# Optimization experiments

Measured on AMD Instinct MI355X. Metric: run time of the kernel, lower is better.

## Reference

```python
import jax, jax.numpy as jnp
import numpy as np

B, S, DMODEL, NHEAD = 2, 2048, 1024, 16
DK = DMODEL // NHEAD
INITRANGE = 0.1


def setup_inputs() -> dict:
    key = jax.random.key(0)
    kq, kk, kv, kwq, kwk, kwv, kwo = jax.random.split(key, 7)
    unif = lambda k, shape: jax.random.uniform(k, shape, jnp.float32, -INITRANGE, INITRANGE)
    return {
        "Q": jax.random.normal(kq, (B, S, DMODEL), jnp.float32),
        "K": jax.random.normal(kk, (B, S, DMODEL), jnp.float32),
        "V": jax.random.normal(kv, (B, S, DMODEL), jnp.float32),
        "WQ": unif(kwq, (NHEAD, DMODEL, DK)),
        "WK": unif(kwk, (NHEAD, DMODEL, DK)),
        "WV": unif(kwv, (NHEAD, DMODEL, DK)),
        "WO": unif(kwo, (NHEAD * DK, DMODEL)),
    }


def reference(Q, K, V, WQ, WK, WV, WO):
    dk = WQ.shape[-1]
    # per-head projections: [B,S,D] x [H,D,dk] -> [B,H,S,dk]
    Qi = jnp.einsum('bsd,hdk->bhsk', Q, WQ)
    Ki = jnp.einsum('bsd,hdk->bhsk', K, WK)
    Vi = jnp.einsum('bsd,hdk->bhsk', V, WV)
    scale = 1.0 / jnp.sqrt(jnp.asarray(dk, Qi.dtype))
    # full attention matrix [B,H,S,S] (faithful to the hand-rolled module; dropout in eval mode)
    attn = jax.nn.softmax(jnp.einsum('bhsk,bhtk->bhst', Qi, Ki) * scale, axis=-1)
    headi = jnp.einsum('bhst,bhtk->bhsk', attn, Vi)  # [B,H,S,dk]
    b, h, s, _ = headi.shape
    # NOTE: original does a raw reshape of contiguous (B,H,S,dk) -> (B,S,H*dk),
    # which mixes head and sequence axes in memory order. jnp row-major reshape
    # reproduces exactly the same element layout.
    out = headi.reshape(b, s, h * dk) @ WO  # [B,S,DMODEL]
    return out
```

## Files before the change

### kernel.cpp

```cpp
#include <hip/hip_runtime.h>
#include <hip/hip_bf16.h>
#include <stdint.h>

typedef unsigned short u16;
typedef unsigned int u32;
typedef __attribute__((ext_vector_type(4))) float f32x4;
typedef __attribute__((ext_vector_type(16))) float f32x16;
typedef __attribute__((ext_vector_type(8))) short bf16x8;
typedef __attribute__((ext_vector_type(4))) unsigned int u32x4;
typedef __attribute__((ext_vector_type(2))) unsigned int u32x2;

#define DEV __device__ __forceinline__

DEV u16 f2bf(float f) {
  union { float f; uint32_t u; } v; v.f = f;
  uint32_t u = v.u;
  return (u16)((u + 0x7fffu + ((u >> 16) & 1u)) >> 16);
}
DEV float bf2f(u16 h) {
  union { uint32_t u; float f; } v; v.u = ((uint32_t)h) << 16;
  return v.f;
}

DEV u32 cvtpk(float a, float b) {
  u32 r;
  asm("v_cvt_pk_bf16_f32 %0, %1, %2" : "=v"(r) : "v"(a), "v"(b));
  return r;
}

DEV void plswap(u32& a, u32& b) {
  asm("v_permlane32_swap_b32 %0, %1" : "+v"(a), "+v"(b));
}

DEV float fexp2(float x) {
  float r;
  asm("v_exp_f32 %0, %1" : "=v"(r) : "v"(x));
  return r;
}

DEV void gload_lds16(const u16* g, u16* l) {
  __builtin_amdgcn_global_load_lds(
      (const __attribute__((address_space(1))) void*)g,
      (__attribute__((address_space(3))) void*)l, 16, 0, 0);
}

__global__ __launch_bounds__(256) void prep_kernel(
    const float* __restrict__ Q, const float* __restrict__ K, const float* __restrict__ V,
    u16* __restrict__ Qb, u16* __restrict__ Kb, u16* __restrict__ Vb) {
  const int i = blockIdx.x * 256 + threadIdx.x;
#pragma unroll
  for (int it = 0; it < 3; ++it) {
    int idx = it * 1048576 + i;
    int which = idx >> 20, j = idx & 1048575;
    const float* src = which == 0 ? Q : (which == 1 ? K : V);
    u16* dst = which == 0 ? Qb : (which == 1 ? Kb : Vb);
    float4 v = ((const float4*)src)[j];
    u32x2 pk;
    pk[0] = (u32)f2bf(v.x) | ((u32)f2bf(v.y) << 16);
    pk[1] = (u32)f2bf(v.z) | ((u32)f2bf(v.w) << 16);
    *(u32x2*)(dst + (size_t)j * 4) = pk;
  }
}

__global__ __launch_bounds__(256) void transposeW_kernel(
    const float* __restrict__ WQ, const float* __restrict__ WK, const float* __restrict__ WV,
    const float* __restrict__ WO, u16* __restrict__ Wt, u16* __restrict__ Wot) {
  __shared__ __align__(16) u16 tl[64][72];
  const int tid = threadIdx.x;
  const int bid = blockIdx.x;
  const float* src;
  u16* dst;
  int rstride;
  if (bid < 768) {
    int p = bid >> 8, rest = bid & 255;
    int h = rest >> 4, dt = rest & 15;
    const float* W = p == 0 ? WQ : (p == 1 ? WK : WV);
    src = W + (size_t)(h * 1024 + dt * 64) * 64;
    dst = Wt + (size_t)p * 1048576 + (size_t)h * 64 * 1024 + dt * 64;
    rstride = 64;
  } else {
    int idx2 = bid - 768;
    int kt = idx2 >> 4, ct = idx2 & 15;
    src = WO + (size_t)kt * 64 * 1024 + ct * 64;
    dst = Wot + (size_t)ct * 64 * 1024 + kt * 64;
    rstride = 1024;
  }
#pragma unroll
  for (int i = 0; i < 2; ++i) {
    int idx = i * 256 + tid;
    int row = idx >> 3, c8 = idx & 7;
    const float* sp = src + (size_t)row * rstride + c8 * 8;
    float4 a = *(const float4*)sp;
    float4 b = *(const float4*)(sp + 4);
    u32x4 pk;
    pk[0] = (u32)f2bf(a.x) | ((u32)f2bf(a.y) << 16);
    pk[1] = (u32)f2bf(a.z) | ((u32)f2bf(a.w) << 16);
    pk[2] = (u32)f2bf(b.x) | ((u32)f2bf(b.y) << 16);
    pk[3] = (u32)f2bf(b.z) | ((u32)f2bf(b.w) << 16);
    *(u32x4*)&tl[row][c8 * 8] = pk;
  }
  __syncthreads();
#pragma unroll
  for (int i = 0; i < 2; ++i) {
    int idx = i * 256 + tid;
    int row2 = idx >> 3, s8 = idx & 7;
    u32x4 outv;
    u16* tp = (u16*)&outv;
#pragma unroll
    for (int j = 0; j < 8; ++j) tp[j] = tl[s8 * 8 + j][row2];
    *(u32x4*)(dst + (size_t)row2 * 1024 + s8 * 8) = outv;
  }
}

template <int OUT_BF16>
__global__ __launch_bounds__(256, 3) void gemm_kernel(const u16* __restrict__ A,
                                                      const u16* __restrict__ Bt,
                                                      void* __restrict__ Cout) {
  __shared__ __align__(16) u16 Alds[128 * 64];
  __shared__ __align__(16) u16 Blds[128 * 64];
  const size_t zo = blockIdx.z;
  A += zo * 4194304;
  Bt += zo * 1048576;
  const int tid = threadIdx.x;
  const int l = tid & 63, w = tid >> 6;
  const int wm = w >> 1, wn = w & 1;
  const int d = blockIdx.x + 32 * blockIdx.y;
  const int orig = (d & 7) * 32 + (d >> 3);
  const int tileM = (orig & 31) * 128, tileN = (orig >> 5) * 128;
  const int lr = l >> 3, lch = l & 7;

  f32x4 acc[4][4] = {};

  for (int kt = 0; kt < 16; ++kt) {
    const int k0 = kt * 64;
#pragma unroll
    for (int i = 0; i < 4; ++i) {
      int r = i * 32 + w * 8 + lr;
      int sch = lch ^ (r & 7);
      gload_lds16(A + (size_t)(tileM + r) * 1024 + k0 + sch * 8, Alds + i * 2048 + w * 512);
      gload_lds16(Bt + (size_t)(tileN + r) * 1024 + k0 + sch * 8, Blds + i * 2048 + w * 512);
    }
    __syncthreads();
    bf16x8 af[4][2], bfr[4][2];
#pragma unroll
    for (int m = 0; m < 4; ++m) {
#pragma unroll
      for (int kk = 0; kk < 2; ++kk) {
        int row = wm * 64 + m * 16 + (l & 15);
        int ch = ((l >> 4) + kk * 4) ^ (row & 7);
        af[m][kk] = *(const bf16x8*)(Alds + row * 64 + ch * 8);
        int rowb = wn * 64 + m * 16 + (l & 15);
        int chb = ((l >> 4) + kk * 4) ^ (rowb & 7);
        bfr[m][kk] = *(const bf16x8*)(Blds + rowb * 64 + chb * 8);
      }
    }
#pragma unroll
    for (int m = 0; m < 4; ++m)
#pragma unroll
      for (int n = 0; n < 4; ++n)
#pragma unroll
        for (int kk = 0; kk < 2; ++kk)
          acc[m][n] = __builtin_amdgcn_mfma_f32_16x16x32_bf16(af[m][kk], bfr[n][kk], acc[m][n], 0, 0, 0);
    __syncthreads();
  }
#pragma unroll
  for (int m = 0; m < 4; ++m) {
    int row0 = tileM + wm * 64 + m * 16 + ((l >> 4) << 2);
#pragma unroll
    for (int n = 0; n < 4; ++n) {
      int col = tileN + wn * 64 + n * 16 + (l & 15);
#pragma unroll
      for (int q = 0; q < 4; ++q) {
        if (OUT_BF16)
          ((u16*)Cout)[zo * 4194304 + (size_t)(row0 + q) * 1024 + col] = f2bf(acc[m][n][q]);
        else
          ((float*)Cout)[(size_t)(row0 + q) * 1024 + col] = acc[m][n][q];
      }
    }
  }
}

__global__ __launch_bounds__(256) void transposeV_kernel(const u16* __restrict__ Vi,
                                                         u16* __restrict__ Vt) {
  __shared__ __align__(16) u16 tl[64][72];
  const int tid = threadIdx.x;
  const int st = blockIdx.x * 64;
  const int bh = blockIdx.y;
  const int b = bh >> 4, h = bh & 15;
#pragma unroll
  for (int i = 0; i < 2; ++i) {
    int idx = i * 256 + tid;
    int s = idx >> 3, ch = idx & 7;
    const u16* src = Vi + (size_t)(b * 2048 + st + s) * 1024 + h * 64 + ch * 8;
    u32x2 a = *(const u32x2*)src;
    u32x2 bb = *(const u32x2*)(src + 4);
    *(u32x2*)&tl[s][ch * 8] = a;
    *(u32x2*)&tl[s][ch * 8 + 4] = bb;
  }
  __syncthreads();
#pragma unroll
  for (int i = 0; i < 2; ++i) {
    int idx = i * 256 + tid;
    int dk = idx >> 3, ch = idx & 7;
    u32x4 outv;
    u16* tp = (u16*)&outv;
#pragma unroll
    for (int j = 0; j < 8; ++j) tp[j] = tl[ch * 8 + j][dk];
    *(u32x4*)(Vt + ((size_t)bh * 64 + dk) * 2048 + st + ch * 8) = outv;
  }
}

__global__ __launch_bounds__(256, 4) void attn_kernel(const u16* __restrict__ Qi,
                                                      const u16* __restrict__ Ki,
                                                      const u16* __restrict__ Vt,
                                                      u16* __restrict__ Op,
                                                      float* __restrict__ Lp) {
  __shared__ __align__(16) u16 Kl[2][4096];
  __shared__ __align__(16) u16 Vl[2][4096];
  const int tid = threadIdx.x;
  const int l = tid & 63, w = tid >> 6;
  const int lq = l & 31, hi = l >> 5;
  const int lr = l >> 3, lch = l & 7;
  const int dd = blockIdx.x;
  const int orig = (dd & 7) * 128 + (dd >> 3);
  const int bh = orig >> 5;
  const int rem = orig & 31;
  const int qb = rem >> 1, kvh = rem & 1;
  const int b = bh >> 4, h = bh & 15;
  const int qt = qb * 128 + w * 32;
  const int tb = kvh * 1024;

  const u16* Kbase = Ki + (size_t)b * 2048 * 1024 + h * 64;
  const u16* Vbase = Vt + (size_t)bh * 64 * 2048;

  bf16x8 qf[4];
  {
    const u16* qp = Qi + (size_t)(b * 2048 + qt + lq) * 1024 + h * 64 + hi * 8;
#pragma unroll
    for (int s = 0; s < 4; ++s) {
      u32x4 t4 = *(const u32x4*)(qp + s * 16);
      u16* tp = (u16*)&t4;
#pragma unroll
      for (int j = 0; j < 8; ++j) tp[j] = f2bf(bf2f(tp[j]) * 0.1803368867f);
      qf[s] = *(bf16x8*)&t4;
    }
  }

  f32x16 o0 = {}, o1 = {};
  float l_r = 0.f;

  auto STAGE = [&](int bb, int t) {
#pragma unroll
    for (int i = 0; i < 2; ++i) {
      int r = i * 32 + w * 8 + lr;
      int sch = lch ^ (r & 7);
      gload_lds16(Kbase + (size_t)(tb + t * 64 + r) * 1024 + sch * 8,
                  Kl[bb] + i * 2048 + w * 512);
      gload_lds16(Vbase + (size_t)r * 2048 + tb + t * 64 + sch * 8,
                  Vl[bb] + i * 2048 + w * 512);
    }
  };

  STAGE(0, 0);

#pragma unroll 2
  for (int tile = 0; tile < 16; ++tile) {
    const int cur = tile & 1;
    __syncthreads();
    if (tile + 1 < 16) STAGE(cur ^ 1, tile + 1);
    const u16* kl = Kl[cur];
    const u16* vl = Vl[cur];

    f32x16 s0 = {}, s1 = {};
    __builtin_amdgcn_s_setprio(1);
#pragma unroll
    for (int s = 0; s < 4; ++s) {
      int row = lq, c = s * 2 + hi;
      bf16x8 kf = *(const bf16x8*)(kl + row * 64 + (c ^ (row & 7)) * 8);
      s0 = __builtin_amdgcn_mfma_f32_32x32x16_bf16(kf, qf[s], s0, 0, 0, 0);
    }
#pragma unroll
    for (int s = 0; s < 4; ++s) {
      int row = 32 + lq, c = s * 2 + hi;
      bf16x8 kf = *(const bf16x8*)(kl + row * 64 + (c ^ (row & 7)) * 8);
      s1 = __builtin_amdgcn_mfma_f32_32x32x16_bf16(kf, qf[s], s1, 0, 0, 0);
    }
    __builtin_amdgcn_s_setprio(0);

    float rs = 0.f;
    bf16x8 pa[4];
#pragma unroll
    for (int s4 = 0; s4 < 4; ++s4) {
      const int rb = 8 * (s4 & 1);
      float p[8];
#pragma unroll
      for (int j = 0; j < 8; ++j) {
        float sv = (s4 < 2) ? ((const float*)&s0)[rb + j] : ((const float*)&s1)[rb + j];
        p[j] = fexp2(sv);
      }
      rs += ((p[0] + p[1]) + (p[2] + p[3])) + ((p[4] + p[5]) + (p[6] + p[7]));
      u32 w10 = cvtpk(p[0], p[1]);
      u32 w11 = cvtpk(p[2], p[3]);
      u32 w20 = cvtpk(p[4], p[5]);
      u32 w21 = cvtpk(p[6], p[7]);
      plswap(w10, w20);
      plswap(w11, w21);
      u32x4 af;
      af[0] = w10;
      af[1] = w11;
      af[2] = w20;
      af[3] = w21;
      pa[s4] = *(bf16x8*)&af;
    }
    rs += __shfl_xor(rs, 32, 64);
    l_r += rs;

    __builtin_amdgcn_s_setprio(1);
#pragma unroll
    for (int s4 = 0; s4 < 4; ++s4) {
      int rowd = lq, c = s4 * 2 + hi;
      bf16x8 vf = *(const bf16x8*)(vl + rowd * 64 + (c ^ (rowd & 7)) * 8);
      o0 = __builtin_amdgcn_mfma_f32_32x32x16_bf16(pa[s4], vf, o0, 0, 0, 0);
    }
#pragma unroll
    for (int s4 = 0; s4 < 4; ++s4) {
      int rowd = 32 + lq, c = s4 * 2 + hi;
      bf16x8 vf = *(const bf16x8*)(vl + rowd * 64 + (c ^ (rowd & 7)) * 8);
      o1 = __builtin_amdgcn_mfma_f32_32x32x16_bf16(pa[s4], vf, o1, 0, 0, 0);
    }
    __builtin_amdgcn_s_setprio(0);
  }

#pragma unroll
  for (int r = 0; r < 16; ++r) {
    int qr = (r & 3) + 8 * (r >> 2) + 4 * hi;
    u16* hp = Op + (size_t)kvh * 4194304 + ((size_t)bh * 2048 + qt + qr) * 64;
    hp[lq] = f2bf(o0[r]);
    hp[32 + lq] = f2bf(o1[r]);
  }
  if (hi == 0) Lp[(size_t)kvh * 65536 + (size_t)bh * 2048 + qt + lq] = l_r;
}

__global__ __launch_bounds__(256) void combine_kernel(const u16* __restrict__ Op,
                                                      const float* __restrict__ Lp,
                                                      u16* __restrict__ Hd) {
  const int idx = blockIdx.x * 256 + threadIdx.x;
  const int g = idx >> 3, j = idx & 7;
  const float fac = 1.f / (Lp[g] + Lp[65536 + g]);
  const size_t off = (size_t)g * 64 + j * 8;
  u32x4 va = *(const u32x4*)(Op + off);
  u32x4 vb = *(const u32x4*)(Op + 4194304 + off);
  const u16* pa = (const u16*)&va;
  const u16* pb = (const u16*)&vb;
  u32x4 outv;
  u16* po = (u16*)&outv;
#pragma unroll
  for (int e = 0; e < 8; ++e) po[e] = f2bf((bf2f(pa[e]) + bf2f(pb[e])) * fac);
  *(u32x4*)(Hd + off) = outv;
}

extern "C" void kernel_launch(void* const* d_in, const int* in_sizes, int n_in,
                              void* d_out, int out_size, void* d_ws, size_t ws_size,
                              hipStream_t stream) {
  const float* Q = (const float*)d_in[0];
  const float* K = (const float*)d_in[1];
  const float* V = (const float*)d_in[2];
  const float* WQ = (const float*)d_in[3];
  const float* WK = (const float*)d_in[4];
  const float* WV = (const float*)d_in[5];
  const float* WO = (const float*)d_in[6];
  float* out = (float*)d_out;

  size_t off = 0;
  char* ws = (char*)d_ws;
  auto nxt = [&](size_t n) { void* p = ws + off; off += (n + 255) & ~(size_t)255; return p; };
  u16* Qb = (u16*)nxt(3ull * 4096 * 1024 * 2);
  u16* Qi = (u16*)nxt(3ull * 4096 * 1024 * 2);
  u16* Vtb = (u16*)nxt(4096ull * 1024 * 2);
  u16* Hd = (u16*)nxt(4096ull * 1024 * 2);
  u16* Wt = (u16*)nxt(3ull * 1048576 * 2);
  u16* Wot = (u16*)nxt(1048576ull * 2);
  float* Lp = (float*)nxt(2ull * 65536 * 4);
  u16* Ki = Qi + 4194304;
  u16* Vi = Qi + 2 * 4194304;
  u16* Op = Qb;

  prep_kernel<<<4096, 256, 0, stream>>>(Q, K, V, Qb, Qb + 4194304, Qb + 2 * 4194304);

  transposeW_kernel<<<1024, 256, 0, stream>>>(WQ, WK, WV, WO, Wt, Wot);

  gemm_kernel<1><<<dim3(32, 8, 3), 256, 0, stream>>>(Qb, Wt, Qi);

  transposeV_kernel<<<dim3(32, 32), 256, 0, stream>>>(Vi, Vtb);

  attn_kernel<<<1024, 256, 0, stream>>>(Qi, Ki, Vtb, Op, Lp);

  combine_kernel<<<2048, 256, 0, stream>>>(Op, Lp, Hd);

  gemm_kernel<0><<<dim3(32, 8, 1), 256, 0, stream>>>(Hd, Wot, out);
}
```

Baseline: 132.9 us.

## Fuse prep with weight transpose and write V transposed from projection GEMM

Merges the input bf16 conversion and weight transpose into one launch, and removes the separate V transpose kernel by having the projection GEMM store the V head directly in the transposed [b,h,dk,s] layout. The goal is fewer kernel launches and no extra round trip of the V projection through memory. The direct transposed store is an uncoalesced 2-byte scatter with stride 2048 elements, which may cost more than the removed kernel saved. The attention kernel's occupancy hint is also raised from 4 to 5 blocks.

```diff
diff --git a/kernel.cpp b/kernel.cpp
--- a/kernel.cpp
+++ b/kernel.cpp
@@ -44,30 +44,31 @@
       (__attribute__((address_space(3))) void*)l, 16, 0, 0);
 }
 
-__global__ __launch_bounds__(256) void prep_kernel(
+__global__ __launch_bounds__(256) void prep_tw_kernel(
     const float* __restrict__ Q, const float* __restrict__ K, const float* __restrict__ V,
-    u16* __restrict__ Qb, u16* __restrict__ Kb, u16* __restrict__ Vb) {
-  const int i = blockIdx.x * 256 + threadIdx.x;
-#pragma unroll
-  for (int it = 0; it < 3; ++it) {
-    int idx = it * 1048576 + i;
-    int which = idx >> 20, j = idx & 1048575;
-    const float* src = which == 0 ? Q : (which == 1 ? K : V);
-    u16* dst = which == 0 ? Qb : (which == 1 ? Kb : Vb);
-    float4 v = ((const float4*)src)[j];
-    u32x2 pk;
-    pk[0] = (u32)f2bf(v.x) | ((u32)f2bf(v.y) << 16);
-    pk[1] = (u32)f2bf(v.z) | ((u32)f2bf(v.w) << 16);
-    *(u32x2*)(dst + (size_t)j * 4) = pk;
-  }
-}
-
-__global__ __launch_bounds__(256) void transposeW_kernel(
     const float* __restrict__ WQ, const float* __restrict__ WK, const float* __restrict__ WV,
-    const float* __restrict__ WO, u16* __restrict__ Wt, u16* __restrict__ Wot) {
+    const float* __restrict__ WO,
+    u16* __restrict__ Qb, u16* __restrict__ Kb, u16* __restrict__ Vb,
+    u16* __restrict__ Wt, u16* __restrict__ Wot) {
   __shared__ __align__(16) u16 tl[64][72];
   const int tid = threadIdx.x;
-  const int bid = blockIdx.x;
+  if (blockIdx.x < 4096) {
+    const int i = blockIdx.x * 256 + tid;
+#pragma unroll
+    for (int it = 0; it < 3; ++it) {
+      int idx = it * 1048576 + i;
+      int which = idx >> 20, j = idx & 1048575;
+      const float* src = which == 0 ? Q : (which == 1 ? K : V);
+      u16* dst = which == 0 ? Qb : (which == 1 ? Kb : Vb);
+      float4 v = ((const float4*)src)[j];
+      u32x2 pk;
+      pk[0] = (u32)f2bf(v.x) | ((u32)f2bf(v.y) << 16);
+      pk[1] = (u32)f2bf(v.z) | ((u32)f2bf(v.w) << 16);
+      *(u32x2*)(dst + (size_t)j * 4) = pk;
+    }
+    return;
+  }
+  const int bid = blockIdx.x - 4096;
   const float* src;
   u16* dst;
   int rstride;
@@ -115,7 +116,8 @@
 template <int OUT_BF16>
 __global__ __launch_bounds__(256, 3) void gemm_kernel(const u16* __restrict__ A,
                                                       const u16* __restrict__ Bt,
-                                                      void* __restrict__ Cout) {
+                                                      void* __restrict__ Cout,
+                                                      u16* __restrict__ VtOut) {
   __shared__ __align__(16) u16 Alds[128 * 64];
   __shared__ __align__(16) u16 Blds[128 * 64];
   const size_t zo = blockIdx.z;
@@ -171,46 +173,25 @@
       int col = tileN + wn * 64 + n * 16 + (l & 15);
 #pragma unroll
       for (int q = 0; q < 4; ++q) {
-        if (OUT_BF16)
-          ((u16*)Cout)[zo * 4194304 + (size_t)(row0 + q) * 1024 + col] = f2bf(acc[m][n][q]);
-        else
+        if (OUT_BF16) {
+          u16 val = f2bf(acc[m][n][q]);
+          if (zo == 2) {
+            int g = row0 + q;
+            int bq = g >> 11, s = g & 2047;
+            int hh = col >> 6, dk = col & 63;
+            VtOut[((((size_t)bq << 4) + hh) * 64 + dk) * 2048 + s] = val;
+          } else {
+            ((u16*)Cout)[zo * 4194304 + (size_t)(row0 + q) * 1024 + col] = val;
+          }
+        } else {
           ((float*)Cout)[(size_t)(row0 + q) * 1024 + col] = acc[m][n][q];
+        }
       }
     }
   }
 }
 
-__global__ __launch_bounds__(256) void transposeV_kernel(const u16* __restrict__ Vi,
-                                                         u16* __restrict__ Vt) {
-  __shared__ __align__(16) u16 tl[64][72];
-  const int tid = threadIdx.x;
-  const int st = blockIdx.x * 64;
-  const int bh = blockIdx.y;
-  const int b = bh >> 4, h = bh & 15;
-#pragma unroll
-  for (int i = 0; i < 2; ++i) {
-    int idx = i * 256 + tid;
-    int s = idx >> 3, ch = idx & 7;
-    const u16* src = Vi + (size_t)(b * 2048 + st + s) * 1024 + h * 64 + ch * 8;
-    u32x2 a = *(const u32x2*)src;
-    u32x2 bb = *(const u32x2*)(src + 4);
-    *(u32x2*)&tl[s][ch * 8] = a;
-    *(u32x2*)&tl[s][ch * 8 + 4] = bb;
-  }
-  __syncthreads();
-#pragma unroll
-  for (int i = 0; i < 2; ++i) {
-    int idx = i * 256 + tid;
-    int dk = idx >> 3, ch = idx & 7;
-    u32x4 outv;
-    u16* tp = (u16*)&outv;
-#pragma unroll
-    for (int j = 0; j < 8; ++j) tp[j] = tl[ch * 8 + j][dk];
-    *(u32x4*)(Vt + ((size_t)bh * 64 + dk) * 2048 + st + ch * 8) = outv;
-  }
-}
-
-__global__ __launch_bounds__(256, 4) void attn_kernel(const u16* __restrict__ Qi,
+__global__ __launch_bounds__(256, 5) void attn_kernel(const u16* __restrict__ Qi,
                                                       const u16* __restrict__ Ki,
                                                       const u16* __restrict__ Vt,
                                                       u16* __restrict__ Op,
@@ -382,20 +363,16 @@
   u16* Wot = (u16*)nxt(1048576ull * 2);
   float* Lp = (float*)nxt(2ull * 65536 * 4);
   u16* Ki = Qi + 4194304;
-  u16* Vi = Qi + 2 * 4194304;
   u16* Op = Qb;
 
-  prep_kernel<<<4096, 256, 0, stream>>>(Q, K, V, Qb, Qb + 4194304, Qb + 2 * 4194304);
-
-  transposeW_kernel<<<1024, 256, 0, stream>>>(WQ, WK, WV, WO, Wt, Wot);
-
-  gemm_kernel<1><<<dim3(32, 8, 3), 256, 0, stream>>>(Qb, Wt, Qi);
-
-  transposeV_kernel<<<dim3(32, 32), 256, 0, stream>>>(Vi, Vtb);
+  prep_tw_kernel<<<5120, 256, 0, stream>>>(Q, K, V, WQ, WK, WV, WO, Qb, Qb + 4194304,
+                                           Qb + 2 * 4194304, Wt, Wot);
+
+  gemm_kernel<1><<<dim3(32, 8, 3), 256, 0, stream>>>(Qb, Wt, Qi, Vtb);
 
   attn_kernel<<<1024, 256, 0, stream>>>(Qi, Ki, Vtb, Op, Lp);
 
   combine_kernel<<<2048, 256, 0, stream>>>(Op, Lp, Hd);
 
-  gemm_kernel<0><<<dim3(32, 8, 1), 256, 0, stream>>>(Hd, Wot, out);
-}
+  gemm_kernel<0><<<dim3(32, 8, 1), 256, 0, stream>>>(Hd, Wot, out, nullptr);
+}
```

Result: slower. 185.3 us (+39.4%).
